# Kernel tuning notes

Measured on AMD Instinct MI355X. Metric: run time of the kernel, lower is better.

The kernel has to match this reference:

```python
import jax, jax.numpy as jnp
import numpy as np

N, E, D, K, B = 50000, 600000, 128, 8, 64
E_DIM = 16  # edge_attr feature dim (hard-coded nn.Linear(16, in_dim))


def setup_inputs() -> dict:
    key = jax.random.key(0)
    ks = jax.random.split(key, 10)
    x = jax.random.normal(ks[0], (N, D), dtype=jnp.float32)
    edge_index = jax.random.randint(ks[1], (2, E), 0, N)
    edge_attr = jax.random.normal(ks[2], (E, E_DIM), dtype=jnp.float32)
    # binary pocket membership mask [N, K]
    pkt_mask = (jax.random.uniform(ks[3], (N, K)) < 0.3).astype(jnp.float32)
    batch = jnp.sort(jax.random.randint(ks[4], (N,), 0, B))
    s = 1.0 / np.sqrt(D)
    We = jax.random.normal(ks[5], (E_DIM, D), dtype=jnp.float32) * (1.0 / np.sqrt(E_DIM))
    be = jnp.zeros((D,), jnp.float32)
    W1 = jax.random.normal(ks[6], (D, D), dtype=jnp.float32) * s
    b1 = jnp.zeros((D,), jnp.float32)
    W2 = jax.random.normal(ks[7], (D, D), dtype=jnp.float32) * s
    b2 = jnp.zeros((D,), jnp.float32)
    eps = jnp.zeros((), jnp.float32)  # GINEConv train_eps init 0
    gamma = jnp.ones((D,), jnp.float32)
    beta = jnp.zeros((D,), jnp.float32)
    Wv = jax.random.normal(ks[8], (D, D), dtype=jnp.float32) * s
    bv = jnp.zeros((D,), jnp.float32)
    return {"x": x, "edge_index": edge_index, "edge_attr": edge_attr,
            "pkt_mask": pkt_mask, "batch": batch,
            "We": We, "be": be, "W1": W1, "b1": b1, "W2": W2, "b2": b2,
            "eps": eps, "gamma": gamma, "beta": beta, "Wv": Wv, "bv": bv}


def reference(x, edge_index, edge_attr, pkt_mask, batch,
              We, be, W1, b1, W2, b2, eps, gamma, beta, Wv, bv):
    src, dst = edge_index[0], edge_index[1]
    # edge_lin: [E,16] -> [E,D]
    edge_emb = edge_attr @ We + be
    # GINEConv: message = relu(x_src + edge_emb), scatter-add at dst
    msg = jax.nn.relu(x[src] + edge_emb)
    agg = jax.ops.segment_sum(msg, dst, num_segments=N)
    h = (1.0 + eps) * x + agg
    x_res = jax.nn.relu(h @ W1 + b1) @ W2 + b2  # nn MLP
    # virtual feedback: pocket-wise masked mean pooling per graph
    xw = x_res[:, None, :] * pkt_mask[:, :, None]          # [N,K,D]
    pocket_sum = jax.ops.segment_sum(xw.reshape(N, K * D), batch,
                                     num_segments=B).reshape(B, K, D)
    pocket_count = jax.ops.segment_sum(pkt_mask, batch, num_segments=B)  # [B,K]
    pocket_mean = pocket_sum / (pocket_count[:, :, None] + 1e-9)
    pocket_emb = pocket_mean @ Wv + bv                      # [B,K,D]
    node_pe = pocket_emb[batch]                             # gather -> [N,K,D]
    x_res = x_res + (node_pe * pkt_mask[:, :, None]).sum(axis=1)
    # LayerNorm (eps=1e-5, population variance as in torch)
    mu = x_res.mean(axis=-1, keepdims=True)
    var = ((x_res - mu) ** 2).mean(axis=-1, keepdims=True)
    y = (x_res - mu) / jnp.sqrt(var + 1e-5) * gamma + beta
    # ReLU activation; dropout is identity in eval mode
    return jax.nn.relu(y)
```

## Files before the change

kernel.cpp:

```cpp
#include <hip/hip_runtime.h>
#include <hip/hip_bf16.h>
#include <stdint.h>

#define D 128
#define K 8
#define BGRAPH 64
#define CH 64
#define GRP 4

typedef __attribute__((ext_vector_type(8))) short bf16x8;
typedef __attribute__((ext_vector_type(4))) float f32x4;
typedef __attribute__((ext_vector_type(2))) float f32x2;

__device__ __forceinline__ short f2bf(float f) {
    union { float f; uint32_t u; } v; v.f = f;
    const uint32_t r = (v.u + 0x7fffu + ((v.u >> 16) & 1u)) >> 16;
    return (short)r;
}
__device__ __forceinline__ float bflo(uint32_t u) {
    union { uint32_t u; float f; } v; v.u = u << 16; return v.f;
}
__device__ __forceinline__ float bfhi(uint32_t u) {
    union { uint32_t u; float f; } v; v.u = u & 0xffff0000u; return v.f;
}

__global__ __launch_bounds__(256) void prep_kernel(
    const float* __restrict__ x, const float* __restrict__ ea,
    const float* __restrict__ W1, const float* __restrict__ W2,
    const float* __restrict__ We, const float* __restrict__ be,
    const int* __restrict__ dst,
    __hip_bfloat16* __restrict__ xb, short* __restrict__ eab,
    short* __restrict__ wb1t, short* __restrict__ wb2t,
    short* __restrict__ webt,
    int* __restrict__ deg,
    int NX, int NEA, int E, int NBX, int NBE, int NBW)
{
    const int b = blockIdx.x;
    const int t = threadIdx.x;
    if (b < NBX) {
        const int i = b * 2048 + t * 8;
        if (i + 8 <= NX) {
            const float4 a = *(const float4*)(x + i);
            const float4 c = *(const float4*)(x + i + 4);
            short v[8];
            v[0] = f2bf(a.x); v[1] = f2bf(a.y); v[2] = f2bf(a.z); v[3] = f2bf(a.w);
            v[4] = f2bf(c.x); v[5] = f2bf(c.y); v[6] = f2bf(c.z); v[7] = f2bf(c.w);
            *(uint4*)((short*)xb + i) = *(const uint4*)v;
        }
    } else if (b < NBX + NBE) {
        const int i = (b - NBX) * 2048 + t * 8;
        if (i + 8 <= NEA) {
            const float4 a = *(const float4*)(ea + i);
            const float4 c = *(const float4*)(ea + i + 4);
            short v[8];
            v[0] = f2bf(a.x); v[1] = f2bf(a.y); v[2] = f2bf(a.z); v[3] = f2bf(a.w);
            v[4] = f2bf(c.x); v[5] = f2bf(c.y); v[6] = f2bf(c.z); v[7] = f2bf(c.w);
            *(uint4*)(eab + i) = *(const uint4*)v;
        }
    } else if (b < NBX + NBE + NBW) {
        const int idx = (b - NBX - NBE) * 256 + t;
        if (idx < 2 * D * D) {
            const int which = idx >> 14;
            const int rem = idx & 16383;
            const int n = rem >> 7;
            const int k = rem & 127;
            const float* W = which ? W2 : W1;
            short* O = which ? wb2t : wb1t;
            O[n * D + k] = f2bf(W[(size_t)k * D + n]);
        } else {
            const int widx = idx - 2 * D * D;
            const int h = widx >> 12;
            const int c = (widx >> 5) & 127;
            const int k = widx & 31;
            float val = 0.f;
            if (k < 16) val = We[k * D + c];
            else if (k == 16) val = be[c];
            const short hi = f2bf(val);
            short outv;
            if (h == 0) outv = hi;
            else {
                union { uint32_t u; float f; } fh;
                fh.u = ((uint32_t)(unsigned short)hi) << 16;
                outv = f2bf(val - fh.f);
            }
            webt[(h << 12) + c * 32 + k] = outv;
        }
    } else {
        const int i = ((b - NBX - NBE - NBW) * 256 + t) * 4;
        if (i + 4 <= E) {
            const int4 v = *(const int4*)(dst + i);
            atomicAdd(&deg[v.x], 1);
            atomicAdd(&deg[v.y], 1);
            atomicAdd(&deg[v.z], 1);
            atomicAdd(&deg[v.w], 1);
        } else {
            for (int j = i; j < E; ++j) atomicAdd(&deg[dst[j]], 1);
        }
    }
}

__global__ __launch_bounds__(256) void scan_partial_kernel(
    const int* __restrict__ deg, int* __restrict__ bsum, int N)
{
    const int t = threadIdx.x;
    const int base = (blockIdx.x * 256 + t) * 4;
    int s = 0;
    if (base + 4 <= N) {
        const int4 v = *(const int4*)(deg + base);
        s = v.x + v.y + v.z + v.w;
    } else {
        for (int j = base; j < N; ++j) s += deg[j];
    }
    __shared__ int red[256];
    red[t] = s;
    __syncthreads();
    for (int off = 128; off; off >>= 1) {
        if (t < off) red[t] += red[t + off];
        __syncthreads();
    }
    if (t == 0) bsum[blockIdx.x] = red[0];
}

__global__ __launch_bounds__(64) void scan_top_kernel(
    const int* __restrict__ bsum, int* __restrict__ boffs, int nb)
{
    __shared__ int sh[64];
    const int t = threadIdx.x;
    const int v = (t < nb) ? bsum[t] : 0;
    sh[t] = v;
    __syncthreads();
    for (int off = 1; off < 64; off <<= 1) {
        const int u = (t >= off) ? sh[t - off] : 0;
        __syncthreads();
        sh[t] += u;
        __syncthreads();
    }
    if (t < nb) boffs[t] = sh[t] - v;
}

__global__ __launch_bounds__(256) void scan_final_kernel(
    const int* __restrict__ deg, const int* __restrict__ boffs,
    int* __restrict__ cursor, int N)
{
    const int t = threadIdx.x;
    const int base = (blockIdx.x * 256 + t) * 4;
    int v0 = 0, v1 = 0, v2 = 0, v3 = 0;
    if (base + 4 <= N) {
        const int4 v = *(const int4*)(deg + base);
        v0 = v.x; v1 = v.y; v2 = v.z; v3 = v.w;
    } else {
        if (base     < N) v0 = deg[base];
        if (base + 1 < N) v1 = deg[base + 1];
        if (base + 2 < N) v2 = deg[base + 2];
        if (base + 3 < N) v3 = deg[base + 3];
    }
    const int s = v0 + v1 + v2 + v3;
    __shared__ int sh[256];
    sh[t] = s;
    __syncthreads();
    for (int off = 1; off < 256; off <<= 1) {
        const int u = (t >= off) ? sh[t - off] : 0;
        __syncthreads();
        sh[t] += u;
        __syncthreads();
    }
    int ex = boffs[blockIdx.x] + sh[t] - s;
    if (base < N)     { cursor[base]     = ex; } ex += v0;
    if (base + 1 < N) { cursor[base + 1] = ex; } ex += v1;
    if (base + 2 < N) { cursor[base + 2] = ex; } ex += v2;
    if (base + 3 < N) { cursor[base + 3] = ex; }
}

__global__ __launch_bounds__(256) void scatter_kernel(
    const int* __restrict__ src, const int* __restrict__ dst,
    int* __restrict__ cursor, uint2* __restrict__ md, int E)
{
    const int i = blockIdx.x * 256 + threadIdx.x;
    if (i < E) {
        const unsigned sv = (unsigned)src[i];
        const unsigned dv = (unsigned)dst[i];
        const int p = atomicAdd(&cursor[dv], 1);
        md[p] = make_uint2(sv | (dv << 16), (unsigned)i);
    }
}

__device__ __forceinline__ void flush_row(
    float* __restrict__ agg, int node, int d, f32x2 acc, int first, int last)
{
    float* p = agg + (size_t)node * D + d;
    if (node == first || node == last) {
        if (acc.x != 0.f) atomicAdd(p,     acc.x);
        if (acc.y != 0.f) atomicAdd(p + 1, acc.y);
    } else {
        *(f32x2*)p = acc;
    }
}

__global__ __launch_bounds__(256) void gine_reduce_kernel(
    const __hip_bfloat16* __restrict__ xb, const uint2* __restrict__ md,
    const short* __restrict__ eab, const short* __restrict__ webt,
    float* __restrict__ agg, int E)
{
    __shared__ float lsh[4][16 * 132];
    const int wave = threadIdx.x >> 6;
    const int lane = threadIdx.x & 63;
    const int chunk = __builtin_amdgcn_readfirstlane(blockIdx.x * 4 + wave);
    const int e0 = chunk * CH;
    if (e0 >= E) return;
    const int d = lane * 2;
    const int m = lane & 15;
    const int q = lane >> 4;
    float* myl = lsh[wave];
    const int NG = CH / GRP;
    const unsigned* mdu = (const unsigned*)md;

    bf16x8 bH[8], bL[8];
    #pragma unroll
    for (int ct = 0; ct < 8; ++ct) {
        bH[ct] = *(const bf16x8*)(webt +        (ct * 16 + m) * 32 + q * 8);
        bL[ct] = *(const bf16x8*)(webt + 4096 + (ct * 16 + m) * 32 + q * 8);
    }

    uint4 afcur = *(const uint4*)(eab +
        (size_t)mdu[2 * (e0 + m) + 1] * 16 + (q & 1) * 8);

    uint2 ma[GRP], mb[GRP], mc[GRP];
    #pragma unroll
    for (int j = 0; j < GRP; ++j) ma[j] = md[e0 + j];
    #pragma unroll
    for (int j = 0; j < GRP; ++j) mb[j] = md[e0 + GRP + j];
    #pragma unroll
    for (int j = 0; j < GRP; ++j) mc[j] = md[e0 + 2 * GRP + j];

    uint32_t xcur[GRP], xn1[GRP];
    #pragma unroll
    for (int j = 0; j < GRP; ++j)
        xcur[j] = *(const uint32_t*)(xb + (size_t)(ma[j].x & 0xffffu) * D + d);
    #pragma unroll
    for (int j = 0; j < GRP; ++j)
        xn1[j] = *(const uint32_t*)(xb + (size_t)(mb[j].x & 0xffffu) * D + d);

    const int first = (int)(ma[0].x >> 16);
    const int last  = (int)(md[e0 + CH - 1].x >> 16);

    f32x2 acc = {0.f, 0.f};
    int cur = first;

    for (int g = 0; g < NG; ++g) {
        if ((g & 3) == 0) {
            const int mg = g >> 2;
            uint4 afn = make_uint4(0u, 0u, 0u, 0u);
            if (mg < 3)
                afn = *(const uint4*)(eab +
                    (size_t)mdu[2 * (e0 + (mg + 1) * 16 + m) + 1] * 16 +
                    (q & 1) * 8);
            uint4 au = afcur;
            if (q >= 2)
                au = make_uint4(q == 2 ? 0x3f80u : 0u, 0u, 0u, 0u);
            const bf16x8 a = *(const bf16x8*)&au;
            f32x4 mm[8];
            #pragma unroll
            for (int ct = 0; ct < 8; ++ct) {
                const f32x4 z = {0.f, 0.f, 0.f, 0.f};
                mm[ct] = __builtin_amdgcn_mfma_f32_16x16x32_bf16(a, bL[ct], z, 0, 0, 0);
            }
            #pragma unroll
            for (int ct = 0; ct < 8; ++ct)
                mm[ct] = __builtin_amdgcn_mfma_f32_16x16x32_bf16(a, bH[ct], mm[ct], 0, 0, 0);
            #pragma unroll
            for (int ct = 0; ct < 8; ++ct)
                #pragma unroll
                for (int r = 0; r < 4; ++r)
                    myl[(q * 4 + r) * 132 + ct * 16 + m] = mm[ct][r];
            afcur = afn;
        }

        uint2 mnew[GRP] = {};
        uint32_t xn2[GRP] = {};
        if (g + 3 < NG) {
            #pragma unroll
            for (int j = 0; j < GRP; ++j) mnew[j] = md[e0 + (g + 3) * GRP + j];
        }
        if (g + 2 < NG) {
            #pragma unroll
            for (int j = 0; j < GRP; ++j)
                xn2[j] = *(const uint32_t*)(xb + (size_t)(mc[j].x & 0xffffu) * D + d);
        }

        #pragma unroll
        for (int j = 0; j < GRP; ++j) {
            const int dk = (int)(ma[j].x >> 16);
            if (dk != cur) {
                flush_row(agg, cur, d, acc, first, last);
                acc.x = 0.f; acc.y = 0.f;
                cur = dk;
            }
            const uint32_t xu = xcur[j];
            const float2 em = *(const float2*)(myl + ((g & 3) * GRP + j) * 132 + d);
            const float m0 = em.x + bflo(xu);
            const float m1 = em.y + bfhi(xu);
            acc.x += m0 > 0.f ? m0 : 0.f;
            acc.y += m1 > 0.f ? m1 : 0.f;
        }

        #pragma unroll
        for (int j = 0; j < GRP; ++j) {
            ma[j] = mb[j]; mb[j] = mc[j]; mc[j] = mnew[j];
            xcur[j] = xn1[j]; xn1[j] = xn2[j];
        }
    }
    flush_row(agg, cur, d, acc, first, last);
}

#define MROWS 64
#define HSTR  132
__global__ __launch_bounds__(256) void mlp_mfma_kernel(
    const float* __restrict__ x, const float* __restrict__ agg,
    const float* __restrict__ epsp,
    const short* __restrict__ wb1t, const float* __restrict__ b1,
    const short* __restrict__ wb2t, const float* __restrict__ b2,
    float* __restrict__ xres, int N)
{
    __shared__ float hsh[MROWS * HSTR];
    const int row0 = blockIdx.x * MROWS;
    const float ep = 1.0f + epsp[0];

    for (int i = threadIdx.x; i < MROWS * D / 4; i += 256) {
        const int flat = i * 4;
        const int r = flat >> 7;
        const int c = flat & (D - 1);
        const int row = row0 + r;
        float4 hv = make_float4(0.f, 0.f, 0.f, 0.f);
        if (row < N) {
            const float4 xv = *(const float4*)(x   + (size_t)row * D + c);
            const float4 av = *(const float4*)(agg + (size_t)row * D + c);
            hv = make_float4(ep * xv.x + av.x, ep * xv.y + av.y,
                             ep * xv.z + av.z, ep * xv.w + av.w);
        }
        *(float4*)(hsh + r * HSTR + c) = hv;
    }
    __syncthreads();

    const int lane = threadIdx.x & 63;
    const int wrow = (threadIdx.x >> 6) * 16;
    const int m = lane & 15;
    const int q = lane >> 4;

    f32x4 acc[8];

    #pragma unroll
    for (int ct = 0; ct < 8; ++ct) {
        const float b = b1[ct * 16 + m];
        acc[ct] = (f32x4){b, b, b, b};
    }
    #pragma unroll
    for (int ks = 0; ks < 4; ++ks) {
        const float* ap = hsh + (wrow + m) * HSTR + ks * 32 + q * 8;
        float av[8];
        *(float4*)(av)     = *(const float4*)ap;
        *(float4*)(av + 4) = *(const float4*)(ap + 4);
        bf16x8 a;
        #pragma unroll
        for (int j = 0; j < 8; ++j) a[j] = f2bf(av[j]);
        #pragma unroll
        for (int ct = 0; ct < 8; ++ct) {
            const bf16x8 b = *(const bf16x8*)(wb1t + (ct * 16 + m) * D + ks * 32 + q * 8);
            acc[ct] = __builtin_amdgcn_mfma_f32_16x16x32_bf16(a, b, acc[ct], 0, 0, 0);
        }
    }
    #pragma unroll
    for (int ct = 0; ct < 8; ++ct)
        #pragma unroll
        for (int r = 0; r < 4; ++r) {
            const float v = acc[ct][r];
            hsh[(wrow + q * 4 + r) * HSTR + ct * 16 + m] = v > 0.f ? v : 0.f;
        }

    #pragma unroll
    for (int ct = 0; ct < 8; ++ct) {
        const float b = b2[ct * 16 + m];
        acc[ct] = (f32x4){b, b, b, b};
    }
    #pragma unroll
    for (int ks = 0; ks < 4; ++ks) {
        const float* ap = hsh + (wrow + m) * HSTR + ks * 32 + q * 8;
        float av[8];
        *(float4*)(av)     = *(const float4*)ap;
        *(float4*)(av + 4) = *(const float4*)(ap + 4);
        bf16x8 a;
        #pragma unroll
        for (int j = 0; j < 8; ++j) a[j] = f2bf(av[j]);
        #pragma unroll
        for (int ct = 0; ct < 8; ++ct) {
            const bf16x8 b = *(const bf16x8*)(wb2t + (ct * 16 + m) * D + ks * 32 + q * 8);
            acc[ct] = __builtin_amdgcn_mfma_f32_16x16x32_bf16(a, b, acc[ct], 0, 0, 0);
        }
    }
    #pragma unroll
    for (int r = 0; r < 4; ++r) {
        const int row = row0 + wrow + q * 4 + r;
        if (row < N) {
            #pragma unroll
            for (int ct = 0; ct < 8; ++ct)
                xres[(size_t)row * D + ct * 16 + m] = acc[ct][r];
        }
    }
}

#define PPARTS 32
__global__ __launch_bounds__(128) void pocket_sum_kernel(
    const float* __restrict__ xres, const float* __restrict__ pmask,
    const int* __restrict__ batch,
    float* __restrict__ psum, float* __restrict__ pcnt, int N)
{
    const int g = blockIdx.x / PPARTS;
    const int part = blockIdx.x % PPARTS;

    int lo, hi;
    {
        int l = 0, r = N;
        while (l < r) { int m = (l + r) >> 1; if (batch[m] < g) l = m + 1; else r = m; }
        lo = l;
        r = N;
        while (l < r) { int m = (l + r) >> 1; if (batch[m] < g + 1) l = m + 1; else r = m; }
        hi = l;
    }
    const int cnt = hi - lo;
    const int per = (cnt + PPARTS - 1) / PPARTS;
    const int s = lo + part * per;
    const int e = min(s + per, hi);

    const int d = threadIdx.x;
    float acc[K];
    #pragma unroll
    for (int k = 0; k < K; ++k) acc[k] = 0.0f;
    float c = 0.0f;

    for (int n = s; n < e; ++n) {
        const float xv = xres[(size_t)n * D + d];
        const float4 m0 = *(const float4*)(pmask + (size_t)n * K);
        const float4 m1 = *(const float4*)(pmask + (size_t)n * K + 4);
        acc[0] += m0.x * xv; acc[1] += m0.y * xv;
        acc[2] += m0.z * xv; acc[3] += m0.w * xv;
        acc[4] += m1.x * xv; acc[5] += m1.y * xv;
        acc[6] += m1.z * xv; acc[7] += m1.w * xv;
        if (d < K) c += pmask[(size_t)n * K + d];
    }
    #pragma unroll
    for (int k = 0; k < K; ++k)
        atomicAdd(&psum[(size_t)g * (K * D) + k * D + d], acc[k]);
    if (d < K) atomicAdd(&pcnt[g * K + d], c);
}

__global__ __launch_bounds__(128) void pocket_emb_kernel(
    const float* __restrict__ psum, const float* __restrict__ pcnt,
    const float* __restrict__ Wv, const float* __restrict__ bv,
    float* __restrict__ pemb)
{
    __shared__ float smean[K * D];
    __shared__ float scnt[K];
    const int g = blockIdx.x;
    const int d = threadIdx.x;
    if (d < K) scnt[d] = pcnt[g * K + d];
    __syncthreads();
    #pragma unroll
    for (int k = 0; k < K; ++k)
        smean[k * D + d] = psum[(size_t)g * (K * D) + k * D + d] / (scnt[k] + 1e-9f);
    __syncthreads();

    float acc[K];
    const float bvv = bv[d];
    #pragma unroll
    for (int k = 0; k < K; ++k) acc[k] = bvv;
    for (int j = 0; j < D; ++j) {
        const float w = Wv[j * D + d];
        #pragma unroll
        for (int k = 0; k < K; ++k) acc[k] += smean[k * D + j] * w;
    }
    #pragma unroll
    for (int k = 0; k < K; ++k)
        pemb[(size_t)g * (K * D) + k * D + d] = acc[k];
}

__global__ __launch_bounds__(256) void ln_kernel(
    const float* __restrict__ xres, const float* __restrict__ pmask,
    const int* __restrict__ batch, const float* __restrict__ pemb,
    const float* __restrict__ gamma, const float* __restrict__ beta,
    float* __restrict__ out, int N)
{
    const int wave = threadIdx.x >> 6;
    const int lane = threadIdx.x & 63;
    const int n = blockIdx.x * 4 + wave;
    if (n >= N) return;
    const int d = lane * 2;

    float2 v = *(const float2*)(xres + (size_t)n * D + d);
    const int g = batch[n];
    const float* pe = pemb + (size_t)g * (K * D);
    const float4 m0 = *(const float4*)(pmask + (size_t)n * K);
    const float4 m1 = *(const float4*)(pmask + (size_t)n * K + 4);
    const float mk[K] = {m0.x, m0.y, m0.z, m0.w, m1.x, m1.y, m1.z, m1.w};
    #pragma unroll
    for (int k = 0; k < K; ++k) {
        if (mk[k] != 0.0f) {
            const float2 p = *(const float2*)(pe + k * D + d);
            v.x += mk[k] * p.x;
            v.y += mk[k] * p.y;
        }
    }

    float s = v.x + v.y;
    #pragma unroll
    for (int off = 32; off; off >>= 1) s += __shfl_xor(s, off, 64);
    const float mu = s * (1.0f / 128.0f);
    const float d0 = v.x - mu, d1 = v.y - mu;
    float sq = d0 * d0 + d1 * d1;
    #pragma unroll
    for (int off = 32; off; off >>= 1) sq += __shfl_xor(sq, off, 64);
    const float var = sq * (1.0f / 128.0f);
    const float inv = rsqrtf(var + 1e-5f);

    const float2 gm = *(const float2*)(gamma + d);
    const float2 bt = *(const float2*)(beta + d);
    float y0 = d0 * inv * gm.x + bt.x;
    float y1 = d1 * inv * gm.y + bt.y;
    y0 = y0 > 0.0f ? y0 : 0.0f;
    y1 = y1 > 0.0f ? y1 : 0.0f;
    *(float2*)(out + (size_t)n * D + d) = make_float2(y0, y1);
}

extern "C" void kernel_launch(void* const* d_in, const int* in_sizes, int n_in,
                              void* d_out, int out_size, void* d_ws, size_t ws_size,
                              hipStream_t stream)
{
    const float* x     = (const float*)d_in[0];
    const int*   ei    = (const int*)  d_in[1];
    const float* ea    = (const float*)d_in[2];
    const float* pmask = (const float*)d_in[3];
    const int*   batch = (const int*)  d_in[4];
    const float* We    = (const float*)d_in[5];
    const float* be    = (const float*)d_in[6];
    const float* W1    = (const float*)d_in[7];
    const float* b1    = (const float*)d_in[8];
    const float* W2    = (const float*)d_in[9];
    const float* b2    = (const float*)d_in[10];
    const float* epsp  = (const float*)d_in[11];
    const float* gamma = (const float*)d_in[12];
    const float* beta  = (const float*)d_in[13];
    const float* Wv    = (const float*)d_in[14];
    const float* bv    = (const float*)d_in[15];
    float* out = (float*)d_out;

    const int N = in_sizes[0] / D;
    const int E = in_sizes[1] / 2;
    const int* src = ei;
    const int* dst = ei + E;

    int*   deg  = (int*)d_ws;
    float* agg  = (float*)(deg + N);
    float* psum = agg + (size_t)N * D;
    float* pcnt = psum + (size_t)BGRAPH * K * D;
    float* xres = pcnt + (size_t)BGRAPH * K;
    float* pemb = xres + (size_t)N * D;
    float* extra = pemb + (size_t)BGRAPH * K * D;
    __hip_bfloat16* xb = (__hip_bfloat16*)(extra + 128);
    short* wb1t = (short*)(xb + (size_t)N * D);
    short* wb2t = wb1t + (size_t)D * D;
    short* webt = wb2t + (size_t)D * D;

    int*   cursor = (int*)xres;
    uint2* md  = (uint2*)(((uintptr_t)(cursor + N) + 15) & ~(uintptr_t)15);
    short* eab = (short*)(md + E);

    int*  bsum  = (int*)extra;
    int*  boffs = bsum + 64;

    const int nb = (N + 1023) / 1024;
    const int nchunks = (E + CH - 1) / CH;
    const int NX = N * D, NEA = E * 16;
    const int NBX = NX / 2048;
    const int NBE = (NEA / 8 + 255) / 256;
    const int NBW = (2 * D * D + 2 * 128 * 32) / 256;
    const int NBH = (E / 4 + 255) / 256;

    const size_t zero_bytes =
        ((size_t)N + (size_t)N * D + (size_t)BGRAPH * K * D + BGRAPH * K) * sizeof(float);
    hipMemsetAsync(d_ws, 0, zero_bytes, stream);

    prep_kernel<<<NBX + NBE + NBW + NBH, 256, 0, stream>>>(
        x, ea, W1, W2, We, be, dst, xb, eab, wb1t, wb2t, webt, deg,
        NX, NEA, E, NBX, NBE, NBW);
    scan_partial_kernel<<<nb, 256, 0, stream>>>(deg, bsum, N);
    scan_top_kernel<<<1, 64, 0, stream>>>(bsum, boffs, nb);
    scan_final_kernel<<<nb, 256, 0, stream>>>(deg, boffs, cursor, N);
    scatter_kernel<<<(E + 255) / 256, 256, 0, stream>>>(src, dst, cursor, md, E);
    gine_reduce_kernel<<<(nchunks + 3) / 4, 256, 0, stream>>>(
        xb, md, eab, webt, agg, E);

    mlp_mfma_kernel<<<(N + MROWS - 1) / MROWS, 256, 0, stream>>>(
        x, agg, epsp, wb1t, b1, wb2t, b2, xres, N);
    pocket_sum_kernel<<<BGRAPH * PPARTS, 128, 0, stream>>>(
        xres, pmask, batch, psum, pcnt, N);
    pocket_emb_kernel<<<BGRAPH, 128, 0, stream>>>(psum, pcnt, Wv, bv, pemb);
    ln_kernel<<<(N + 3) / 4, 256, 0, stream>>>(
        xres, pmask, batch, pemb, gamma, beta, out, N);
}
```

Measured before the change: 359.3 us.

## Read fp32 edge_attr directly in GINE reduce and deepen gather prefetch

Drops the prep pass that converted edge_attr to bf16 and instead loads fp32 edge features inside the gather-reduce kernel, converting them in registers just before the MFMA. This removes a full write and re-read of the bf16 edge_attr buffer, but the random per-edge gather now fetches twice as many bytes. The prefetch pipeline for metadata and x rows is deepened by one stage, and the LDS staging buffer swaps row padding for an XOR swizzle to avoid bank conflicts while using less shared memory.

```diff
diff --git a/kernel.cpp b/kernel.cpp
--- a/kernel.cpp
+++ b/kernel.cpp
@@ -25,15 +25,15 @@
 }
 
 __global__ __launch_bounds__(256) void prep_kernel(
-    const float* __restrict__ x, const float* __restrict__ ea,
+    const float* __restrict__ x,
     const float* __restrict__ W1, const float* __restrict__ W2,
     const float* __restrict__ We, const float* __restrict__ be,
     const int* __restrict__ dst,
-    __hip_bfloat16* __restrict__ xb, short* __restrict__ eab,
+    __hip_bfloat16* __restrict__ xb,
     short* __restrict__ wb1t, short* __restrict__ wb2t,
     short* __restrict__ webt,
     int* __restrict__ deg,
-    int NX, int NEA, int E, int NBX, int NBE, int NBW)
+    int NX, int E, int NBX, int NBW)
 {
     const int b = blockIdx.x;
     const int t = threadIdx.x;
@@ -47,18 +47,8 @@
             v[4] = f2bf(c.x); v[5] = f2bf(c.y); v[6] = f2bf(c.z); v[7] = f2bf(c.w);
             *(uint4*)((short*)xb + i) = *(const uint4*)v;
         }
-    } else if (b < NBX + NBE) {
-        const int i = (b - NBX) * 2048 + t * 8;
-        if (i + 8 <= NEA) {
-            const float4 a = *(const float4*)(ea + i);
-            const float4 c = *(const float4*)(ea + i + 4);
-            short v[8];
-            v[0] = f2bf(a.x); v[1] = f2bf(a.y); v[2] = f2bf(a.z); v[3] = f2bf(a.w);
-            v[4] = f2bf(c.x); v[5] = f2bf(c.y); v[6] = f2bf(c.z); v[7] = f2bf(c.w);
-            *(uint4*)(eab + i) = *(const uint4*)v;
-        }
-    } else if (b < NBX + NBE + NBW) {
-        const int idx = (b - NBX - NBE) * 256 + t;
+    } else if (b < NBX + NBW) {
+        const int idx = (b - NBX) * 256 + t;
         if (idx < 2 * D * D) {
             const int which = idx >> 14;
             const int rem = idx & 16383;
@@ -86,7 +76,7 @@
             webt[(h << 12) + c * 32 + k] = outv;
         }
     } else {
-        const int i = ((b - NBX - NBE - NBW) * 256 + t) * 4;
+        const int i = ((b - NBX - NBW) * 256 + t) * 4;
         if (i + 4 <= E) {
             const int4 v = *(const int4*)(dst + i);
             atomicAdd(&deg[v.x], 1);
@@ -198,10 +188,10 @@
 
 __global__ __launch_bounds__(256) void gine_reduce_kernel(
     const __hip_bfloat16* __restrict__ xb, const uint2* __restrict__ md,
-    const short* __restrict__ eab, const short* __restrict__ webt,
+    const float* __restrict__ ea, const short* __restrict__ webt,
     float* __restrict__ agg, int E)
 {
-    __shared__ float lsh[4][16 * 132];
+    __shared__ float lsh[4][16 * 128];
     const int wave = threadIdx.x >> 6;
     const int lane = threadIdx.x & 63;
     const int chunk = __builtin_amdgcn_readfirstlane(blockIdx.x * 4 + wave);
@@ -213,6 +203,7 @@
     float* myl = lsh[wave];
     const int NG = CH / GRP;
     const unsigned* mdu = (const unsigned*)md;
+    const int qswz = (q & 1) << 4;
 
     bf16x8 bH[8], bL[8];
     #pragma unroll
@@ -221,26 +212,35 @@
         bL[ct] = *(const bf16x8*)(webt + 4096 + (ct * 16 + m) * 32 + q * 8);
     }
 
-    uint4 afcur = *(const uint4*)(eab +
-        (size_t)mdu[2 * (e0 + m) + 1] * 16 + (q & 1) * 8);
-
-    uint2 ma[GRP], mb[GRP], mc[GRP];
-    #pragma unroll
-    for (int j = 0; j < GRP; ++j) ma[j] = md[e0 + j];
-    #pragma unroll
-    for (int j = 0; j < GRP; ++j) mb[j] = md[e0 + GRP + j];
-    #pragma unroll
-    for (int j = 0; j < GRP; ++j) mc[j] = md[e0 + 2 * GRP + j];
-
-    uint32_t xcur[GRP], xn1[GRP];
+    float4 af0 = {0.f, 0.f, 0.f, 0.f}, af1 = {0.f, 0.f, 0.f, 0.f};
+    if ((q & 2) == 0) {
+        const float* p = ea + (size_t)mdu[2 * (e0 + m) + 1] * 16 + (q & 1) * 8;
+        af0 = *(const float4*)p;
+        af1 = *(const float4*)(p + 4);
+    }
+
+    uint2 m0[GRP], m1g[GRP], m2g[GRP], m3g[GRP];
+    #pragma unroll
+    for (int j = 0; j < GRP; ++j) m0[j]  = md[e0 + j];
+    #pragma unroll
+    for (int j = 0; j < GRP; ++j) m1g[j] = md[e0 + GRP + j];
+    #pragma unroll
+    for (int j = 0; j < GRP; ++j) m2g[j] = md[e0 + 2 * GRP + j];
+    #pragma unroll
+    for (int j = 0; j < GRP; ++j) m3g[j] = md[e0 + 3 * GRP + j];
+
+    uint32_t x0[GRP], x1[GRP], x2[GRP];
     #pragma unroll
     for (int j = 0; j < GRP; ++j)
-        xcur[j] = *(const uint32_t*)(xb + (size_t)(ma[j].x & 0xffffu) * D + d);
+        x0[j] = *(const uint32_t*)(xb + (size_t)(m0[j].x  & 0xffffu) * D + d);
     #pragma unroll
     for (int j = 0; j < GRP; ++j)
-        xn1[j] = *(const uint32_t*)(xb + (size_t)(mb[j].x & 0xffffu) * D + d);
-
-    const int first = (int)(ma[0].x >> 16);
+        x1[j] = *(const uint32_t*)(xb + (size_t)(m1g[j].x & 0xffffu) * D + d);
+    #pragma unroll
+    for (int j = 0; j < GRP; ++j)
+        x2[j] = *(const uint32_t*)(xb + (size_t)(m2g[j].x & 0xffffu) * D + d);
+
+    const int first = (int)(m0[0].x >> 16);
     const int last  = (int)(md[e0 + CH - 1].x >> 16);
 
     f32x2 acc = {0.f, 0.f};
@@ -249,15 +249,23 @@
     for (int g = 0; g < NG; ++g) {
         if ((g & 3) == 0) {
             const int mg = g >> 2;
-            uint4 afn = make_uint4(0u, 0u, 0u, 0u);
-            if (mg < 3)
-                afn = *(const uint4*)(eab +
+            float4 an0 = {0.f, 0.f, 0.f, 0.f}, an1 = {0.f, 0.f, 0.f, 0.f};
+            if (mg < 3 && (q & 2) == 0) {
+                const float* p = ea +
                     (size_t)mdu[2 * (e0 + (mg + 1) * 16 + m) + 1] * 16 +
-                    (q & 1) * 8);
-            uint4 au = afcur;
-            if (q >= 2)
-                au = make_uint4(q == 2 ? 0x3f80u : 0u, 0u, 0u, 0u);
-            const bf16x8 a = *(const bf16x8*)&au;
+                    (q & 1) * 8;
+                an0 = *(const float4*)p;
+                an1 = *(const float4*)(p + 4);
+            }
+            bf16x8 a;
+            if (q < 2) {
+                a[0] = f2bf(af0.x); a[1] = f2bf(af0.y);
+                a[2] = f2bf(af0.z); a[3] = f2bf(af0.w);
+                a[4] = f2bf(af1.x); a[5] = f2bf(af1.y);
+                a[6] = f2bf(af1.z); a[7] = f2bf(af1.w);
+            } else {
+                a = (bf16x8){(short)(q == 2 ? 0x3f80 : 0), 0, 0, 0, 0, 0, 0, 0};
+            }
             f32x4 mm[8];
             #pragma unroll
             for (int ct = 0; ct < 8; ++ct) {
@@ -271,42 +279,44 @@
             for (int ct = 0; ct < 8; ++ct)
                 #pragma unroll
                 for (int r = 0; r < 4; ++r)
-                    myl[(q * 4 + r) * 132 + ct * 16 + m] = mm[ct][r];
-            afcur = afn;
+                    myl[(q * 4 + r) * 128 + ((ct * 16 + m) ^ qswz)] = mm[ct][r];
+            af0 = an0; af1 = an1;
         }
 
         uint2 mnew[GRP] = {};
-        uint32_t xn2[GRP] = {};
+        uint32_t xn[GRP] = {};
+        if (g + 4 < NG) {
+            #pragma unroll
+            for (int j = 0; j < GRP; ++j) mnew[j] = md[e0 + (g + 4) * GRP + j];
+        }
         if (g + 3 < NG) {
             #pragma unroll
-            for (int j = 0; j < GRP; ++j) mnew[j] = md[e0 + (g + 3) * GRP + j];
-        }
-        if (g + 2 < NG) {
-            #pragma unroll
             for (int j = 0; j < GRP; ++j)
-                xn2[j] = *(const uint32_t*)(xb + (size_t)(mc[j].x & 0xffffu) * D + d);
+                xn[j] = *(const uint32_t*)(xb + (size_t)(m3g[j].x & 0xffffu) * D + d);
         }
 
         #pragma unroll
         for (int j = 0; j < GRP; ++j) {
-            const int dk = (int)(ma[j].x >> 16);
+            const int dk = (int)(m0[j].x >> 16);
             if (dk != cur) {
                 flush_row(agg, cur, d, acc, first, last);
                 acc.x = 0.f; acc.y = 0.f;
                 cur = dk;
             }
-            const uint32_t xu = xcur[j];
-            const float2 em = *(const float2*)(myl + ((g & 3) * GRP + j) * 132 + d);
-            const float m0 = em.x + bflo(xu);
-            const float m1 = em.y + bfhi(xu);
-            acc.x += m0 > 0.f ? m0 : 0.f;
-            acc.y += m1 > 0.f ? m1 : 0.f;
+            const uint32_t xu = x0[j];
+            const int el = (g & 3) * GRP + j;
+            const float2 em = *(const float2*)(myl + el * 128 +
+                                               (d ^ ((el & 4) << 2)));
+            const float v0 = em.x + bflo(xu);
+            const float v1 = em.y + bfhi(xu);
+            acc.x += v0 > 0.f ? v0 : 0.f;
+            acc.y += v1 > 0.f ? v1 : 0.f;
         }
 
         #pragma unroll
         for (int j = 0; j < GRP; ++j) {
-            ma[j] = mb[j]; mb[j] = mc[j]; mc[j] = mnew[j];
-            xcur[j] = xn1[j]; xn1[j] = xn2[j];
+            m0[j] = m1g[j]; m1g[j] = m2g[j]; m2g[j] = m3g[j]; m3g[j] = mnew[j];
+            x0[j] = x1[j]; x1[j] = x2[j]; x2[j] = xn[j];
         }
     }
     flush_row(agg, cur, d, acc, first, last);
@@ -570,16 +580,14 @@
 
     int*   cursor = (int*)xres;
     uint2* md  = (uint2*)(((uintptr_t)(cursor + N) + 15) & ~(uintptr_t)15);
-    short* eab = (short*)(md + E);
 
     int*  bsum  = (int*)extra;
     int*  boffs = bsum + 64;
 
     const int nb = (N + 1023) / 1024;
     const int nchunks = (E + CH - 1) / CH;
-    const int NX = N * D, NEA = E * 16;
+    const int NX = N * D;
     const int NBX = NX / 2048;
-    const int NBE = (NEA / 8 + 255) / 256;
     const int NBW = (2 * D * D + 2 * 128 * 32) / 256;
     const int NBH = (E / 4 + 255) / 256;
 
@@ -587,15 +595,15 @@
         ((size_t)N + (size_t)N * D + (size_t)BGRAPH * K * D + BGRAPH * K) * sizeof(float);
     hipMemsetAsync(d_ws, 0, zero_bytes, stream);
 
-    prep_kernel<<<NBX + NBE + NBW + NBH, 256, 0, stream>>>(
-        x, ea, W1, W2, We, be, dst, xb, eab, wb1t, wb2t, webt, deg,
-        NX, NEA, E, NBX, NBE, NBW);
+    prep_kernel<<<NBX + NBW + NBH, 256, 0, stream>>>(
+        x, W1, W2, We, be, dst, xb, wb1t, wb2t, webt, deg,
+        NX, E, NBX, NBW);
     scan_partial_kernel<<<nb, 256, 0, stream>>>(deg, bsum, N);
     scan_top_kernel<<<1, 64, 0, stream>>>(bsum, boffs, nb);
     scan_final_kernel<<<nb, 256, 0, stream>>>(deg, boffs, cursor, N);
     scatter_kernel<<<(E + 255) / 256, 256, 0, stream>>>(src, dst, cursor, md, E);
     gine_reduce_kernel<<<(nchunks + 3) / 4, 256, 0, stream>>>(
-        xb, md, eab, webt, agg, E);
+        xb, md, ea, webt, agg, E);
 
     mlp_mfma_kernel<<<(N + MROWS - 1) / MROWS, 256, 0, stream>>>(
         x, agg, epsp, wb1t, b1, wb2t, b2, xres, N);
```

New measurement: 358.5 us. No clear change (-0.2%).

## Convert edge_attr to bf16 in scatter order to remove indirect gather

Applied to the files above, without the earlier changes.

The fp32-to-bf16 conversion of edge attributes moves from the prep kernel into the scatter kernel, which writes each converted row at its CSR-sorted position. The reduce kernel can then read edge attributes contiguously by sorted index instead of doing a dependent load of the original edge id followed by a random gather. In exchange, the scatter kernel now issues scattered 32-byte writes, and the conversion work runs in a later, serial stage instead of in parallel with the prep kernel.

```diff
diff --git a/kernel.cpp b/kernel.cpp
--- a/kernel.cpp
+++ b/kernel.cpp
@@ -25,15 +25,15 @@
 }
 
 __global__ __launch_bounds__(256) void prep_kernel(
-    const float* __restrict__ x, const float* __restrict__ ea,
+    const float* __restrict__ x,
     const float* __restrict__ W1, const float* __restrict__ W2,
     const float* __restrict__ We, const float* __restrict__ be,
     const int* __restrict__ dst,
-    __hip_bfloat16* __restrict__ xb, short* __restrict__ eab,
+    __hip_bfloat16* __restrict__ xb,
     short* __restrict__ wb1t, short* __restrict__ wb2t,
     short* __restrict__ webt,
     int* __restrict__ deg,
-    int NX, int NEA, int E, int NBX, int NBE, int NBW)
+    int NX, int E, int NBX, int NBW)
 {
     const int b = blockIdx.x;
     const int t = threadIdx.x;
@@ -47,18 +47,8 @@
             v[4] = f2bf(c.x); v[5] = f2bf(c.y); v[6] = f2bf(c.z); v[7] = f2bf(c.w);
             *(uint4*)((short*)xb + i) = *(const uint4*)v;
         }
-    } else if (b < NBX + NBE) {
-        const int i = (b - NBX) * 2048 + t * 8;
-        if (i + 8 <= NEA) {
-            const float4 a = *(const float4*)(ea + i);
-            const float4 c = *(const float4*)(ea + i + 4);
-            short v[8];
-            v[0] = f2bf(a.x); v[1] = f2bf(a.y); v[2] = f2bf(a.z); v[3] = f2bf(a.w);
-            v[4] = f2bf(c.x); v[5] = f2bf(c.y); v[6] = f2bf(c.z); v[7] = f2bf(c.w);
-            *(uint4*)(eab + i) = *(const uint4*)v;
-        }
-    } else if (b < NBX + NBE + NBW) {
-        const int idx = (b - NBX - NBE) * 256 + t;
+    } else if (b < NBX + NBW) {
+        const int idx = (b - NBX) * 256 + t;
         if (idx < 2 * D * D) {
             const int which = idx >> 14;
             const int rem = idx & 16383;
@@ -86,7 +76,7 @@
             webt[(h << 12) + c * 32 + k] = outv;
         }
     } else {
-        const int i = ((b - NBX - NBE - NBW) * 256 + t) * 4;
+        const int i = ((b - NBX - NBW) * 256 + t) * 4;
         if (i + 4 <= E) {
             const int4 v = *(const int4*)(dst + i);
             atomicAdd(&deg[v.x], 1);
@@ -173,7 +163,9 @@
 
 __global__ __launch_bounds__(256) void scatter_kernel(
     const int* __restrict__ src, const int* __restrict__ dst,
-    int* __restrict__ cursor, uint2* __restrict__ md, int E)
+    const float* __restrict__ ea,
+    int* __restrict__ cursor, uint2* __restrict__ md,
+    short* __restrict__ eabs, int E)
 {
     const int i = blockIdx.x * 256 + threadIdx.x;
     if (i < E) {
@@ -181,6 +173,16 @@
         const unsigned dv = (unsigned)dst[i];
         const int p = atomicAdd(&cursor[dv], 1);
         md[p] = make_uint2(sv | (dv << 16), (unsigned)i);
+        const float4* ep = (const float4*)(ea + (size_t)i * 16);
+        const float4 a = ep[0], b = ep[1], c = ep[2], e4 = ep[3];
+        short v[16];
+        v[0]  = f2bf(a.x);  v[1]  = f2bf(a.y);  v[2]  = f2bf(a.z);  v[3]  = f2bf(a.w);
+        v[4]  = f2bf(b.x);  v[5]  = f2bf(b.y);  v[6]  = f2bf(b.z);  v[7]  = f2bf(b.w);
+        v[8]  = f2bf(c.x);  v[9]  = f2bf(c.y);  v[10] = f2bf(c.z);  v[11] = f2bf(c.w);
+        v[12] = f2bf(e4.x); v[13] = f2bf(e4.y); v[14] = f2bf(e4.z); v[15] = f2bf(e4.w);
+        uint4* op = (uint4*)(eabs + (size_t)p * 16);
+        op[0] = *(const uint4*)v;
+        op[1] = *(const uint4*)(v + 8);
     }
 }
 
@@ -198,7 +200,7 @@
 
 __global__ __launch_bounds__(256) void gine_reduce_kernel(
     const __hip_bfloat16* __restrict__ xb, const uint2* __restrict__ md,
-    const short* __restrict__ eab, const short* __restrict__ webt,
+    const short* __restrict__ eabs, const short* __restrict__ webt,
     float* __restrict__ agg, int E)
 {
     __shared__ float lsh[4][16 * 132];
@@ -212,7 +214,6 @@
     const int q = lane >> 4;
     float* myl = lsh[wave];
     const int NG = CH / GRP;
-    const unsigned* mdu = (const unsigned*)md;
 
     bf16x8 bH[8], bL[8];
     #pragma unroll
@@ -221,8 +222,7 @@
         bL[ct] = *(const bf16x8*)(webt + 4096 + (ct * 16 + m) * 32 + q * 8);
     }
 
-    uint4 afcur = *(const uint4*)(eab +
-        (size_t)mdu[2 * (e0 + m) + 1] * 16 + (q & 1) * 8);
+    uint4 afcur = *(const uint4*)(eabs + (size_t)(e0 + m) * 16 + (q & 1) * 8);
 
     uint2 ma[GRP], mb[GRP], mc[GRP];
     #pragma unroll
@@ -251,9 +251,8 @@
             const int mg = g >> 2;
             uint4 afn = make_uint4(0u, 0u, 0u, 0u);
             if (mg < 3)
-                afn = *(const uint4*)(eab +
-                    (size_t)mdu[2 * (e0 + (mg + 1) * 16 + m) + 1] * 16 +
-                    (q & 1) * 8);
+                afn = *(const uint4*)(eabs +
+                    (size_t)(e0 + (mg + 1) * 16 + m) * 16 + (q & 1) * 8);
             uint4 au = afcur;
             if (q >= 2)
                 au = make_uint4(q == 2 ? 0x3f80u : 0u, 0u, 0u, 0u);
@@ -275,11 +274,11 @@
             afcur = afn;
         }
 
-        uint2 mnew[GRP] = {};
+        uint2 mnn[GRP] = {};
         uint32_t xn2[GRP] = {};
         if (g + 3 < NG) {
             #pragma unroll
-            for (int j = 0; j < GRP; ++j) mnew[j] = md[e0 + (g + 3) * GRP + j];
+            for (int j = 0; j < GRP; ++j) mnn[j] = md[e0 + (g + 3) * GRP + j];
         }
         if (g + 2 < NG) {
             #pragma unroll
@@ -297,15 +296,15 @@
             }
             const uint32_t xu = xcur[j];
             const float2 em = *(const float2*)(myl + ((g & 3) * GRP + j) * 132 + d);
-            const float m0 = em.x + bflo(xu);
-            const float m1 = em.y + bfhi(xu);
-            acc.x += m0 > 0.f ? m0 : 0.f;
-            acc.y += m1 > 0.f ? m1 : 0.f;
+            const float v0 = em.x + bflo(xu);
+            const float v1 = em.y + bfhi(xu);
+            acc.x += v0 > 0.f ? v0 : 0.f;
+            acc.y += v1 > 0.f ? v1 : 0.f;
         }
 
         #pragma unroll
         for (int j = 0; j < GRP; ++j) {
-            ma[j] = mb[j]; mb[j] = mc[j]; mc[j] = mnew[j];
+            ma[j] = mb[j]; mb[j] = mc[j]; mc[j] = mnn[j];
             xcur[j] = xn1[j]; xn1[j] = xn2[j];
         }
     }
@@ -570,16 +569,15 @@
 
     int*   cursor = (int*)xres;
     uint2* md  = (uint2*)(((uintptr_t)(cursor + N) + 15) & ~(uintptr_t)15);
-    short* eab = (short*)(md + E);
+    short* eabs = (short*)(md + E);
 
     int*  bsum  = (int*)extra;
     int*  boffs = bsum + 64;
 
     const int nb = (N + 1023) / 1024;
     const int nchunks = (E + CH - 1) / CH;
-    const int NX = N * D, NEA = E * 16;
+    const int NX = N * D;
     const int NBX = NX / 2048;
-    const int NBE = (NEA / 8 + 255) / 256;
     const int NBW = (2 * D * D + 2 * 128 * 32) / 256;
     const int NBH = (E / 4 + 255) / 256;
 
@@ -587,15 +585,16 @@
         ((size_t)N + (size_t)N * D + (size_t)BGRAPH * K * D + BGRAPH * K) * sizeof(float);
     hipMemsetAsync(d_ws, 0, zero_bytes, stream);
 
-    prep_kernel<<<NBX + NBE + NBW + NBH, 256, 0, stream>>>(
-        x, ea, W1, W2, We, be, dst, xb, eab, wb1t, wb2t, webt, deg,
-        NX, NEA, E, NBX, NBE, NBW);
+    prep_kernel<<<NBX + NBW + NBH, 256, 0, stream>>>(
+        x, W1, W2, We, be, dst, xb, wb1t, wb2t, webt, deg,
+        NX, E, NBX, NBW);
     scan_partial_kernel<<<nb, 256, 0, stream>>>(deg, bsum, N);
     scan_top_kernel<<<1, 64, 0, stream>>>(bsum, boffs, nb);
     scan_final_kernel<<<nb, 256, 0, stream>>>(deg, boffs, cursor, N);
-    scatter_kernel<<<(E + 255) / 256, 256, 0, stream>>>(src, dst, cursor, md, E);
+    scatter_kernel<<<(E + 255) / 256, 256, 0, stream>>>(
+        src, dst, ea, cursor, md, eabs, E);
     gine_reduce_kernel<<<(nchunks + 3) / 4, 256, 0, stream>>>(
-        xb, md, eab, webt, agg, E);
+        xb, md, eabs, webt, agg, E);
 
     mlp_mfma_kernel<<<(N + MROWS - 1) / MROWS, 256, 0, stream>>>(
         x, agg, epsp, wb1t, b1, wb2t, b2, xres, N);
```

After: 349.4 us. 1.03x faster.
